# Kernel optimization log

Hardware: AMD Instinct MI355X
Metric: run time of the kernel (lower is better)

The kernel has to match this reference:

```python
import jax, jax.numpy as jnp
import numpy as np

N, E = 50000, 400000
HID, HT = 128, 128
HEADS, C = 4, 128  # TransformerConv heads=4, out_channels=hidden_X


def setup_inputs() -> dict:
    key = jax.random.key(0)
    ks = jax.random.split(key, 16)
    s = lambda k, shape, fan: jax.random.normal(k, shape, jnp.float32) / np.sqrt(fan)
    return {
        "edge_index": jax.random.randint(ks[0], (2, E), 0, N, dtype=jnp.int32),
        "h_X": jax.random.normal(ks[1], (N, HID), jnp.float32),
        "h_t": jax.random.normal(ks[2], (1, HT), jnp.float32),
        # TransformerConv params: lin_query/key/value: (HID -> HEADS*C), lin_skip: (HID -> C)
        "Wq": s(ks[3], (HID, HEADS * C), HID), "bq": jnp.zeros((HEADS * C,), jnp.float32),
        "Wk": s(ks[4], (HID, HEADS * C), HID), "bk": jnp.zeros((HEADS * C,), jnp.float32),
        "Wv": s(ks[5], (HID, HEADS * C), HID), "bv": jnp.zeros((HEADS * C,), jnp.float32),
        "Wskip": s(ks[6], (HID, C), HID), "bskip": jnp.zeros((C,), jnp.float32),
        # update_X: Linear(HID+HT -> HID), LayerNorm(HID)
        "Wup": s(ks[7], (HID + HT, HID), HID + HT), "bup": jnp.zeros((HID,), jnp.float32),
        "gamma": jnp.ones((HID,), jnp.float32), "beta": jnp.zeros((HID,), jnp.float32),
    }


def transformer_conv(h_X, edge_index, Wq, bq, Wk, bk, Wv, bv, Wskip, bskip):
    n = h_X.shape[0]
    src, dst = edge_index[0], edge_index[1]  # messages flow src -> dst
    q = (h_X @ Wq + bq).reshape(n, HEADS, C)
    k = (h_X @ Wk + bk).reshape(n, HEADS, C)
    v = (h_X @ Wv + bv).reshape(n, HEADS, C)
    # per-edge attention scores [E, H]
    score = jnp.einsum('ehc,ehc->eh', q[dst], k[src]) / np.sqrt(C)
    # segment softmax over incoming edges of each destination node
    m = jax.ops.segment_max(score, dst, num_segments=n)          # [N, H]
    ex = jnp.exp(score - m[dst])                                 # [E, H]
    denom = jax.ops.segment_sum(ex, dst, num_segments=n)        # [N, H]
    alpha = ex / denom[dst]                                      # [E, H]
    agg = jax.ops.segment_sum(alpha[..., None] * v[src], dst, num_segments=n)  # [N, H, C]
    out = agg.mean(axis=1)                                       # concat=False -> mean over heads
    return out + h_X @ Wskip + bskip                             # root_weight=True


def reference(edge_index, h_X, h_t, Wq, bq, Wk, bk, Wv, bv, Wskip, bskip,
              Wup, bup, gamma, beta):
    n = h_X.shape[0]
    h_att = transformer_conv(h_X, edge_index, Wq, bq, Wk, bk, Wv, bv, Wskip, bskip)
    h_t_exp = jnp.broadcast_to(h_t, (n, h_t.shape[1]))
    h = jnp.concatenate([h_att, h_t_exp], axis=1)
    h = jax.nn.relu(h @ Wup + bup)
    # LayerNorm (eps=1e-5); Dropout is identity in eval
    mu = h.mean(axis=-1, keepdims=True)
    var = ((h - mu) ** 2).mean(axis=-1, keepdims=True)
    return (h - mu) / jnp.sqrt(var + 1e-5) * gamma + beta
```

## Files before the change

### kernel.cpp

```cpp
#include <hip/hip_runtime.h>

typedef unsigned short u16;
typedef unsigned int   u32;

#define HID   128
#define HEADS 4
#define CH    128
#define HC    512
#define UT    32

typedef __bf16 bf16x8v __attribute__((ext_vector_type(8)));
typedef float  f32x4v  __attribute__((ext_vector_type(4)));
union FragU { uint4 u; bf16x8v b; };

static __device__ __forceinline__ float bf2f(u16 u) {
  union { u32 u; float f; } x;
  x.u = ((u32)u) << 16;
  return x.f;
}
static __device__ __forceinline__ u16 f2bf(float f) {
  union { float f; u32 u; } x;
  x.f = f;
  u32 r = x.u + 0x7fffu + ((x.u >> 16) & 1u);
  return (u16)(r >> 16);
}

__global__ void zero_kernel(int* p, int n) {
  int i = blockIdx.x * 256 + threadIdx.x;
  if (i < n) p[i] = 0;
}

__global__ void hist_kernel(const int* dst_idx, int* deg, int E) {
  int e = blockIdx.x * 256 + threadIdx.x;
  if (e < E) atomicAdd(&deg[dst_idx[e]], 1);
}

__global__ void blocksum_kernel(const int* deg, int* bsums, int n) {
  __shared__ int buf[256];
  int i = blockIdx.x * 256 + threadIdx.x;
  int v = 0;
  if (i < n) v = deg[i];
  buf[threadIdx.x] = v;
  __syncthreads();
  for (int off = 128; off > 0; off >>= 1) {
    if (threadIdx.x < off) buf[threadIdx.x] += buf[threadIdx.x + off];
    __syncthreads();
  }
  if (threadIdx.x == 0) bsums[blockIdx.x] = buf[0];
}

__global__ void scanb_kernel(const int* bsums, int* boffs, int nb) {
  __shared__ int buf[256];
  __shared__ int carry_s;
  int tid = threadIdx.x;
  if (tid == 0) carry_s = 0;
  __syncthreads();
  for (int base = 0; base < nb; base += 256) {
    int i = base + tid;
    int v = 0;
    if (i < nb) v = bsums[i];
    buf[tid] = v;
    __syncthreads();
    for (int off = 1; off < 256; off <<= 1) {
      int t = 0;
      if (tid >= off) t = buf[tid - off];
      __syncthreads();
      buf[tid] += t;
      __syncthreads();
    }
    int incl = buf[tid] + carry_s;
    if (i < nb) boffs[i] = incl - v;
    __syncthreads();
    if (tid == 255) carry_s = incl;
    __syncthreads();
  }
}

__global__ void scanfinal_kernel(const int* deg, const int* boffs,
                                 int* row_ptr, int* cursor, int n) {
  __shared__ int buf[256];
  int tid = threadIdx.x;
  int i = blockIdx.x * 256 + tid;
  int v = 0;
  if (i < n) v = deg[i];
  buf[tid] = v;
  __syncthreads();
  for (int off = 1; off < 256; off <<= 1) {
    int t = 0;
    if (tid >= off) t = buf[tid - off];
    __syncthreads();
    buf[tid] += t;
    __syncthreads();
  }
  int incl = buf[tid] + boffs[blockIdx.x];
  if (i < n) {
    row_ptr[i + 1] = incl;
    cursor[i] = incl - v;
  }
  if (i == 0) row_ptr[0] = 0;
}

__global__ void scatter_kernel(const int* src_idx, const int* dst_idx,
                               int* cursor, int* col, int E) {
  int e = blockIdx.x * 256 + threadIdx.x;
  if (e < E) {
    int pos = atomicAdd(&cursor[dst_idx[e]], 1);
    col[pos] = src_idx[e];
  }
}

__global__ void packH_kernel(const float* __restrict__ hX,
                             u16* __restrict__ hpack, int N, int total) {
  int i = blockIdx.x * 256 + threadIdx.x;
  if (i >= total) return;
  int j = i & 7;
  int lane = (i >> 3) & 63;
  int kc = (i >> 9) & 3;
  int ntile = i >> 11;
  int node = ntile * 16 + (lane & 15);
  int k = kc * 32 + (lane >> 4) * 8 + j;
  float v = (node < N) ? hX[(size_t)node * HID + k] : 0.f;
  hpack[i] = f2bf(v);
}

__global__ void packW_kernel(const float* __restrict__ WA,
                             const float* __restrict__ WB, int colsA, int ldA,
                             int ldB, u16* __restrict__ Wp, int total) {
  int i = blockIdx.x * 256 + threadIdx.x;
  if (i >= total) return;
  int j = i & 7;
  int lane = (i >> 3) & 63;
  int kc = (i >> 9) & 3;
  int ct = i >> 11;
  int n = ct * 16 + (lane & 15);
  int k = kc * 32 + (lane >> 4) * 8 + j;
  float w = (n < colsA) ? WA[(size_t)k * ldA + n]
                        : WB[(size_t)k * ldB + (n - colsA)];
  Wp[i] = f2bf(w);
}

__global__ __launch_bounds__(256) void mfma_proj_kernel(
    const u16* __restrict__ hpack, const u16* __restrict__ Wp,
    const float* __restrict__ biasLo, const float* __restrict__ biasHi,
    u16* __restrict__ outLo, u16* __restrict__ outHiB,
    float* __restrict__ outHiF, int hiIsF32, int N) {
  int t = threadIdx.x;
  int wv = t >> 6;
  int L = t & 63;
  int ct = blockIdx.y * 4 + wv;
  int nt0 = blockIdx.x * 4;

  f32x4v acc[4];
  for (int mt = 0; mt < 4; ++mt) acc[mt] = (f32x4v){0.f, 0.f, 0.f, 0.f};

  const u16* wb = Wp + (size_t)ct * 2048;
  const u16* hb = hpack + (size_t)nt0 * 2048;

  for (int kc = 0; kc < 4; ++kc) {
    FragU bf;
    bf.u = *(const uint4*)(wb + kc * 512 + L * 8);
    for (int mt = 0; mt < 4; ++mt) {
      FragU af;
      af.u = *(const uint4*)(hb + mt * 2048 + kc * 512 + L * 8);
      acc[mt] =
          __builtin_amdgcn_mfma_f32_16x16x32_bf16(af.b, bf.b, acc[mt], 0, 0, 0);
    }
  }

  int colq = L & 15;
  int quad = L >> 4;
  int n = ct * 16 + colq;
  float bias = (n < 512) ? biasLo[n] : biasHi[n - 512];
  for (int mt = 0; mt < 4; ++mt) {
    for (int rg = 0; rg < 4; ++rg) {
      int node = (nt0 + mt) * 16 + quad * 4 + rg;
      if (node < N) {
        float val = acc[mt][rg] + bias;
        if (n < 512) {
          outLo[(size_t)node * HC + n] = f2bf(val);
        } else if (hiIsF32) {
          outHiF[(size_t)node * HID + (n - 512)] = val;
        } else {
          outHiB[(size_t)node * HC + (n - 512)] = f2bf(val);
        }
      }
    }
  }
}

__global__ void score_kernel(const u16* qb, const u16* kb, const int* row_ptr,
                             const int* col_src, float* scores, int N) {
  int node = blockIdx.x * 4 + (threadIdx.x >> 6);
  if (node >= N) return;
  int lane = threadIdx.x & 63;
  int head = lane >> 4;
  int r = lane & 15;
  int foff = head * CH + r * 8;

  float qf[8];
  {
    uint4 raw = *(const uint4*)(qb + (size_t)node * HC + foff);
    qf[0] = bf2f((u16)(raw.x & 0xffffu));
    qf[1] = bf2f((u16)(raw.x >> 16));
    qf[2] = bf2f((u16)(raw.y & 0xffffu));
    qf[3] = bf2f((u16)(raw.y >> 16));
    qf[4] = bf2f((u16)(raw.z & 0xffffu));
    qf[5] = bf2f((u16)(raw.z >> 16));
    qf[6] = bf2f((u16)(raw.w & 0xffffu));
    qf[7] = bf2f((u16)(raw.w >> 16));
  }

  int e0 = row_ptr[node];
  int e1 = row_ptr[node + 1];
  for (int e = e0; e < e1; ++e) {
    int s = col_src[e];
    uint4 raw = *(const uint4*)(kb + (size_t)s * HC + foff);
    float p = 0.f;
    p = fmaf(bf2f((u16)(raw.x & 0xffffu)), qf[0], p);
    p = fmaf(bf2f((u16)(raw.x >> 16)),     qf[1], p);
    p = fmaf(bf2f((u16)(raw.y & 0xffffu)), qf[2], p);
    p = fmaf(bf2f((u16)(raw.y >> 16)),     qf[3], p);
    p = fmaf(bf2f((u16)(raw.z & 0xffffu)), qf[4], p);
    p = fmaf(bf2f((u16)(raw.z >> 16)),     qf[5], p);
    p = fmaf(bf2f((u16)(raw.w & 0xffffu)), qf[6], p);
    p = fmaf(bf2f((u16)(raw.w >> 16)),     qf[7], p);
    p += __shfl_xor(p, 1);
    p += __shfl_xor(p, 2);
    p += __shfl_xor(p, 4);
    p += __shfl_xor(p, 8);
    if (r == 0) scores[(size_t)e * HEADS + head] = p * 0.08838834764831845f;
  }
}

__global__ void attn_kernel(const float* scores, const u16* vb,
                            const int* row_ptr, const int* col_src,
                            float* out, int N) {
  int node = blockIdx.x * 4 + (threadIdx.x >> 6);
  if (node >= N) return;
  int lane = threadIdx.x & 63;
  int head = lane >> 4;
  int r = lane & 15;
  int foff = head * CH + r * 8;

  float m = -3.402823466e38f;
  float l = 0.f;
  float acc[8];
  for (int j = 0; j < 8; ++j) acc[j] = 0.f;

  int e0 = row_ptr[node];
  int e1 = row_ptr[node + 1];
  for (int e = e0; e < e1; ++e) {
    float sc = scores[(size_t)e * HEADS + head];
    int s = col_src[e];
    uint4 raw = *(const uint4*)(vb + (size_t)s * HC + foff);
    float vf[8];
    vf[0] = bf2f((u16)(raw.x & 0xffffu));
    vf[1] = bf2f((u16)(raw.x >> 16));
    vf[2] = bf2f((u16)(raw.y & 0xffffu));
    vf[3] = bf2f((u16)(raw.y >> 16));
    vf[4] = bf2f((u16)(raw.z & 0xffffu));
    vf[5] = bf2f((u16)(raw.z >> 16));
    vf[6] = bf2f((u16)(raw.w & 0xffffu));
    vf[7] = bf2f((u16)(raw.w >> 16));
    float mnew = fmaxf(m, sc);
    float scale = expf(m - mnew);
    float pe = expf(sc - mnew);
    l = l * scale + pe;
    for (int j = 0; j < 8; ++j) acc[j] = fmaf(acc[j], scale, pe * vf[j]);
    m = mnew;
  }

  float inv = 0.f;
  if (l > 0.f) inv = 1.0f / l;
  float val[8];
  for (int j = 0; j < 8; ++j) {
    float x = acc[j] * inv;
    x += __shfl_xor(x, 16);
    x += __shfl_xor(x, 32);
    val[j] = x * 0.25f;
  }

  if (head == 0) {
    float* p = out + (size_t)node * HID + r * 8;
    float4 a = *(const float4*)(p);
    float4 b = *(const float4*)(p + 4);
    a.x += val[0]; a.y += val[1]; a.z += val[2]; a.w += val[3];
    b.x += val[4]; b.y += val[5]; b.z += val[6]; b.w += val[7];
    *(float4*)(p) = a;
    *(float4*)(p + 4) = b;
  }
}

__global__ void cvec_kernel(const float* h_t, const float* Wup,
                            const float* bup, float* cvec) {
  int c = threadIdx.x;
  float acc = bup[c];
  for (int k = 0; k < 128; ++k)
    acc = fmaf(h_t[k], Wup[(size_t)(128 + k) * 128 + c], acc);
  cvec[c] = acc;
}

__global__ __launch_bounds__(256) void ATTLayer_19396072308956_kernel(
    float* out, const float* __restrict__ Wup, const float* __restrict__ cvec,
    const float* __restrict__ gamma, const float* __restrict__ beta, int N) {
  __shared__ float Wl[64 * 128];
  __shared__ float Hl[UT * 128];
  int t = threadIdx.x;
  int n0 = blockIdx.x * UT;

  for (int i = t * 4; i < UT * 128; i += 1024) {
    int node = n0 + (i >> 7);
    float4 v;
    if (node < N) {
      v = *(const float4*)(out + (size_t)node * HID + (i & 127));
    } else {
      v.x = 0.f; v.y = 0.f; v.z = 0.f; v.w = 0.f;
    }
    *(float4*)(Hl + i) = v;
  }

  int wv = t >> 6;
  int r = t & 63;
  int c0 = 2 * r;
  float2 cv = *(const float2*)(cvec + c0);
  float a0[8];
  float a1[8];
  for (int j = 0; j < 8; ++j) {
    a0[j] = cv.x;
    a1[j] = cv.y;
  }

  for (int ph = 0; ph < 2; ++ph) {
    __syncthreads();
    for (int i = t * 4; i < 64 * 128; i += 1024) {
      *(float4*)(Wl + i) = *(const float4*)(Wup + (size_t)ph * 64 * 128 + i);
    }
    __syncthreads();
    const float* hbase = Hl + (wv * 8) * 128 + ph * 64;
#pragma unroll 8
    for (int k = 0; k < 64; ++k) {
      float2 w2 = *(const float2*)(Wl + k * 128 + c0);
      for (int j = 0; j < 8; ++j) {
        float h = hbase[j * 128 + k];
        a0[j] = fmaf(h, w2.x, a0[j]);
        a1[j] = fmaf(h, w2.y, a1[j]);
      }
    }
  }

  float2 g = *(const float2*)(gamma + c0);
  float2 b = *(const float2*)(beta + c0);
  for (int j = 0; j < 8; ++j) {
    int node = n0 + wv * 8 + j;
    float r0 = fmaxf(a0[j], 0.f);
    float r1 = fmaxf(a1[j], 0.f);
    float s = r0 + r1;
    for (int msk = 1; msk < 64; msk <<= 1) s += __shfl_xor(s, msk);
    float mean = s * (1.0f / 128.0f);
    float d0 = r0 - mean;
    float d1 = r1 - mean;
    float sq = d0 * d0 + d1 * d1;
    for (int msk = 1; msk < 64; msk <<= 1) sq += __shfl_xor(sq, msk);
    float rstd = rsqrtf(sq * (1.0f / 128.0f) + 1e-5f);
    if (node < N) {
      float2 o;
      o.x = d0 * rstd * g.x + b.x;
      o.y = d1 * rstd * g.y + b.y;
      *(float2*)(out + (size_t)node * HID + c0) = o;
    }
  }
}

extern "C" void kernel_launch(void* const* d_in, const int* in_sizes, int n_in,
                              void* d_out, int out_size, void* d_ws,
                              size_t ws_size, hipStream_t stream) {
  (void)n_in;
  (void)out_size;
  (void)ws_size;

  const int* edge_index = (const int*)d_in[0];
  const float* hX    = (const float*)d_in[1];
  const float* h_t   = (const float*)d_in[2];
  const float* Wq    = (const float*)d_in[3];
  const float* bq    = (const float*)d_in[4];
  const float* Wk    = (const float*)d_in[5];
  const float* bk    = (const float*)d_in[6];
  const float* Wv    = (const float*)d_in[7];
  const float* bv    = (const float*)d_in[8];
  const float* Wskip = (const float*)d_in[9];
  const float* bskip = (const float*)d_in[10];
  const float* Wup   = (const float*)d_in[11];
  const float* bup   = (const float*)d_in[12];
  const float* gamma = (const float*)d_in[13];
  const float* beta  = (const float*)d_in[14];

  const int E = in_sizes[0] / 2;
  const int N = in_sizes[1] / HID;
  const int* src_idx = edge_index;
  const int* dst_idx = edge_index + E;
  const int NB = (N + 255) / 256;
  const int NTILES = (N + 15) / 16;
  const int NTILES4 = ((NTILES + 3) / 4) * 4;

  char* w = (char*)d_ws;
  size_t off = 0;
  float* cvec = (float*)(w + off);
  off += 256 * 4;
  int* deg = (int*)(w + off);
  off += ((size_t)N * 4 + 255) / 256 * 256;
  int* row_ptr = (int*)(w + off);
  off += ((size_t)(N + 1) * 4 + 255) / 256 * 256;
  int* cursor = (int*)(w + off);
  off += ((size_t)N * 4 + 255) / 256 * 256;
  int* bsums = (int*)(w + off);
  off += ((size_t)NB * 4 + 255) / 256 * 256;
  int* boffs = (int*)(w + off);
  off += ((size_t)NB * 4 + 255) / 256 * 256;
  int* col = (int*)(w + off);
  off += ((size_t)E * 4 + 255) / 256 * 256;
  float* scores = (float*)(w + off);
  off += ((size_t)E * HEADS * 4 + 255) / 256 * 256;
  u16* hpack = (u16*)(w + off);
  off += ((size_t)NTILES4 * 2048 * 2 + 255) / 256 * 256;
  u16* Wp1 = (u16*)(w + off);
  off += ((size_t)128 * 1024 * 2 + 255) / 256 * 256;
  u16* Wp2 = (u16*)(w + off);
  off += ((size_t)128 * 640 * 2 + 255) / 256 * 256;
  u16* bigA = (u16*)(w + off);
  off += ((size_t)N * HC * 2 + 255) / 256 * 256;
  u16* bigB = (u16*)(w + off);
  off += ((size_t)N * HC * 2 + 255) / 256 * 256;

  float* out = (float*)d_out;

  zero_kernel<<<NB, 256, 0, stream>>>(deg, N);
  hist_kernel<<<(E + 255) / 256, 256, 0, stream>>>(dst_idx, deg, E);
  blocksum_kernel<<<NB, 256, 0, stream>>>(deg, bsums, N);
  scanb_kernel<<<1, 256, 0, stream>>>(bsums, boffs, NB);
  scanfinal_kernel<<<NB, 256, 0, stream>>>(deg, boffs, row_ptr, cursor, N);
  scatter_kernel<<<(E + 255) / 256, 256, 0, stream>>>(src_idx, dst_idx, cursor,
                                                      col, E);

  int totH = NTILES4 * 2048;
  packH_kernel<<<(totH + 255) / 256, 256, 0, stream>>>(hX, hpack, N, totH);
  packW_kernel<<<(128 * 1024 + 255) / 256, 256, 0, stream>>>(
      Wq, Wk, 512, HC, HC, Wp1, 128 * 1024);
  packW_kernel<<<(128 * 640 + 255) / 256, 256, 0, stream>>>(
      Wv, Wskip, 512, HC, HID, Wp2, 128 * 640);

  cvec_kernel<<<1, 128, 0, stream>>>(h_t, Wup, bup, cvec);

  mfma_proj_kernel<<<dim3(NTILES4 / 4, 16), 256, 0, stream>>>(
      hpack, Wp1, bq, bk, bigA, bigB, (float*)nullptr, 0, N);

  score_kernel<<<(N + 3) / 4, 256, 0, stream>>>(bigA, bigB, row_ptr, col,
                                                scores, N);

  mfma_proj_kernel<<<dim3(NTILES4 / 4, 10), 256, 0, stream>>>(
      hpack, Wp2, bv, bskip, bigA, (u16*)nullptr, out, 1, N);

  attn_kernel<<<(N + 3) / 4, 256, 0, stream>>>(scores, bigA, row_ptr, col, out,
                                               N);

  ATTLayer_19396072308956_kernel<<<(N + UT - 1) / UT, 256, 0, stream>>>(
      out, Wup, cvec, gamma, beta, N);
}
```

Measured before the change: 461.9 us.

## Fuse score and softmax-aggregation into one edge pass with separate V buffer

Adds a fused attention kernel that computes q·k scores and the online-softmax aggregation of v in a single pass over each node's incoming edges, processing two edges per iteration. V is written to a new workspace buffer so Q/K stay live. This drops the per-edge score array write/read and the second walk over the CSR structure. The fused path is used only if the workspace is large enough, and exp is switched to the fast __expf in both paths.

```diff
diff --git a/kernel.cpp b/kernel.cpp
--- a/kernel.cpp
+++ b/kernel.cpp
@@ -23,6 +23,17 @@
   x.f = f;
   u32 r = x.u + 0x7fffu + ((x.u >> 16) & 1u);
   return (u16)(r >> 16);
+}
+
+static __device__ __forceinline__ void unpack8(uint4 raw, float* dst) {
+  dst[0] = bf2f((u16)(raw.x & 0xffffu));
+  dst[1] = bf2f((u16)(raw.x >> 16));
+  dst[2] = bf2f((u16)(raw.y & 0xffffu));
+  dst[3] = bf2f((u16)(raw.y >> 16));
+  dst[4] = bf2f((u16)(raw.z & 0xffffu));
+  dst[5] = bf2f((u16)(raw.z >> 16));
+  dst[6] = bf2f((u16)(raw.w & 0xffffu));
+  dst[7] = bf2f((u16)(raw.w >> 16));
 }
 
 __global__ void zero_kernel(int* p, int n) {
@@ -188,6 +199,112 @@
   }
 }
 
+__global__ void fused_attn_kernel(const u16* __restrict__ qb,
+                                  const u16* __restrict__ kb,
+                                  const u16* __restrict__ vb,
+                                  const int* __restrict__ row_ptr,
+                                  const int* __restrict__ col_src,
+                                  float* out, int N) {
+  int node = blockIdx.x * 4 + (threadIdx.x >> 6);
+  if (node >= N) return;
+  int lane = threadIdx.x & 63;
+  int head = lane >> 4;
+  int r = lane & 15;
+  int foff = head * CH + r * 8;
+  const float sscale = 0.08838834764831845f;
+
+  float qf[8];
+  unpack8(*(const uint4*)(qb + (size_t)node * HC + foff), qf);
+
+  float m = -3.402823466e38f;
+  float l = 0.f;
+  float acc[8];
+  for (int j = 0; j < 8; ++j) acc[j] = 0.f;
+
+  int e0 = row_ptr[node];
+  int e1 = row_ptr[node + 1];
+  int e = e0;
+  for (; e + 2 <= e1; e += 2) {
+    int s0 = col_src[e];
+    int s1 = col_src[e + 1];
+    uint4 k0 = *(const uint4*)(kb + (size_t)s0 * HC + foff);
+    uint4 k1 = *(const uint4*)(kb + (size_t)s1 * HC + foff);
+    uint4 v0 = *(const uint4*)(vb + (size_t)s0 * HC + foff);
+    uint4 v1 = *(const uint4*)(vb + (size_t)s1 * HC + foff);
+    float k0f[8], k1f[8];
+    unpack8(k0, k0f);
+    unpack8(k1, k1f);
+    float p0 = 0.f, p1 = 0.f;
+    for (int j = 0; j < 8; ++j) {
+      p0 = fmaf(k0f[j], qf[j], p0);
+      p1 = fmaf(k1f[j], qf[j], p1);
+    }
+    p0 += __shfl_xor(p0, 1);
+    p1 += __shfl_xor(p1, 1);
+    p0 += __shfl_xor(p0, 2);
+    p1 += __shfl_xor(p1, 2);
+    p0 += __shfl_xor(p0, 4);
+    p1 += __shfl_xor(p1, 4);
+    p0 += __shfl_xor(p0, 8);
+    p1 += __shfl_xor(p1, 8);
+    float sc0 = p0 * sscale;
+    float sc1 = p1 * sscale;
+    float mnew = fmaxf(m, fmaxf(sc0, sc1));
+    float so = __expf(m - mnew);
+    float pe0 = __expf(sc0 - mnew);
+    float pe1 = __expf(sc1 - mnew);
+    l = l * so + pe0 + pe1;
+    float v0f[8], v1f[8];
+    unpack8(v0, v0f);
+    unpack8(v1, v1f);
+    for (int j = 0; j < 8; ++j)
+      acc[j] = fmaf(acc[j], so, fmaf(pe0, v0f[j], pe1 * v1f[j]));
+    m = mnew;
+  }
+  if (e < e1) {
+    int s0 = col_src[e];
+    uint4 k0 = *(const uint4*)(kb + (size_t)s0 * HC + foff);
+    uint4 v0 = *(const uint4*)(vb + (size_t)s0 * HC + foff);
+    float k0f[8];
+    unpack8(k0, k0f);
+    float p0 = 0.f;
+    for (int j = 0; j < 8; ++j) p0 = fmaf(k0f[j], qf[j], p0);
+    p0 += __shfl_xor(p0, 1);
+    p0 += __shfl_xor(p0, 2);
+    p0 += __shfl_xor(p0, 4);
+    p0 += __shfl_xor(p0, 8);
+    float sc0 = p0 * sscale;
+    float mnew = fmaxf(m, sc0);
+    float so = __expf(m - mnew);
+    float pe0 = __expf(sc0 - mnew);
+    l = l * so + pe0;
+    float v0f[8];
+    unpack8(v0, v0f);
+    for (int j = 0; j < 8; ++j) acc[j] = fmaf(acc[j], so, pe0 * v0f[j]);
+    m = mnew;
+  }
+
+  float inv = 0.f;
+  if (l > 0.f) inv = 1.0f / l;
+  float val[8];
+  for (int j = 0; j < 8; ++j) {
+    float x = acc[j] * inv;
+    x += __shfl_xor(x, 16);
+    x += __shfl_xor(x, 32);
+    val[j] = x * 0.25f;
+  }
+
+  if (head == 0) {
+    float* p = out + (size_t)node * HID + r * 8;
+    float4 a = *(const float4*)(p);
+    float4 b = *(const float4*)(p + 4);
+    a.x += val[0]; a.y += val[1]; a.z += val[2]; a.w += val[3];
+    b.x += val[4]; b.y += val[5]; b.z += val[6]; b.w += val[7];
+    *(float4*)(p) = a;
+    *(float4*)(p + 4) = b;
+  }
+}
+
 __global__ void score_kernel(const u16* qb, const u16* kb, const int* row_ptr,
                              const int* col_src, float* scores, int N) {
   int node = blockIdx.x * 4 + (threadIdx.x >> 6);
@@ -198,32 +315,17 @@
   int foff = head * CH + r * 8;
 
   float qf[8];
-  {
-    uint4 raw = *(const uint4*)(qb + (size_t)node * HC + foff);
-    qf[0] = bf2f((u16)(raw.x & 0xffffu));
-    qf[1] = bf2f((u16)(raw.x >> 16));
-    qf[2] = bf2f((u16)(raw.y & 0xffffu));
-    qf[3] = bf2f((u16)(raw.y >> 16));
-    qf[4] = bf2f((u16)(raw.z & 0xffffu));
-    qf[5] = bf2f((u16)(raw.z >> 16));
-    qf[6] = bf2f((u16)(raw.w & 0xffffu));
-    qf[7] = bf2f((u16)(raw.w >> 16));
-  }
+  unpack8(*(const uint4*)(qb + (size_t)node * HC + foff), qf);
 
   int e0 = row_ptr[node];
   int e1 = row_ptr[node + 1];
   for (int e = e0; e < e1; ++e) {
     int s = col_src[e];
     uint4 raw = *(const uint4*)(kb + (size_t)s * HC + foff);
+    float kf[8];
+    unpack8(raw, kf);
     float p = 0.f;
-    p = fmaf(bf2f((u16)(raw.x & 0xffffu)), qf[0], p);
-    p = fmaf(bf2f((u16)(raw.x >> 16)),     qf[1], p);
-    p = fmaf(bf2f((u16)(raw.y & 0xffffu)), qf[2], p);
-    p = fmaf(bf2f((u16)(raw.y >> 16)),     qf[3], p);
-    p = fmaf(bf2f((u16)(raw.z & 0xffffu)), qf[4], p);
-    p = fmaf(bf2f((u16)(raw.z >> 16)),     qf[5], p);
-    p = fmaf(bf2f((u16)(raw.w & 0xffffu)), qf[6], p);
-    p = fmaf(bf2f((u16)(raw.w >> 16)),     qf[7], p);
+    for (int j = 0; j < 8; ++j) p = fmaf(kf[j], qf[j], p);
     p += __shfl_xor(p, 1);
     p += __shfl_xor(p, 2);
     p += __shfl_xor(p, 4);
@@ -254,17 +356,10 @@
     int s = col_src[e];
     uint4 raw = *(const uint4*)(vb + (size_t)s * HC + foff);
     float vf[8];
-    vf[0] = bf2f((u16)(raw.x & 0xffffu));
-    vf[1] = bf2f((u16)(raw.x >> 16));
-    vf[2] = bf2f((u16)(raw.y & 0xffffu));
-    vf[3] = bf2f((u16)(raw.y >> 16));
-    vf[4] = bf2f((u16)(raw.z & 0xffffu));
-    vf[5] = bf2f((u16)(raw.z >> 16));
-    vf[6] = bf2f((u16)(raw.w & 0xffffu));
-    vf[7] = bf2f((u16)(raw.w >> 16));
+    unpack8(raw, vf);
     float mnew = fmaxf(m, sc);
-    float scale = expf(m - mnew);
-    float pe = expf(sc - mnew);
+    float scale = __expf(m - mnew);
+    float pe = __expf(sc - mnew);
     l = l * scale + pe;
     for (int j = 0; j < 8; ++j) acc[j] = fmaf(acc[j], scale, pe * vf[j]);
     m = mnew;
@@ -376,7 +471,6 @@
                               size_t ws_size, hipStream_t stream) {
   (void)n_in;
   (void)out_size;
-  (void)ws_size;
 
   const int* edge_index = (const int*)d_in[0];
   const float* hX    = (const float*)d_in[1];
@@ -430,6 +524,9 @@
   off += ((size_t)N * HC * 2 + 255) / 256 * 256;
   u16* bigB = (u16*)(w + off);
   off += ((size_t)N * HC * 2 + 255) / 256 * 256;
+  u16* bigC = (u16*)(w + off);
+  size_t off_fused = off + ((size_t)N * HC * 2 + 255) / 256 * 256;
+  const int use_fused = (ws_size >= off_fused) ? 1 : 0;
 
   float* out = (float*)d_out;
 
@@ -453,14 +550,19 @@
   mfma_proj_kernel<<<dim3(NTILES4 / 4, 16), 256, 0, stream>>>(
       hpack, Wp1, bq, bk, bigA, bigB, (float*)nullptr, 0, N);
 
-  score_kernel<<<(N + 3) / 4, 256, 0, stream>>>(bigA, bigB, row_ptr, col,
-                                                scores, N);
-
-  mfma_proj_kernel<<<dim3(NTILES4 / 4, 10), 256, 0, stream>>>(
-      hpack, Wp2, bv, bskip, bigA, (u16*)nullptr, out, 1, N);
-
-  attn_kernel<<<(N + 3) / 4, 256, 0, stream>>>(scores, bigA, row_ptr, col, out,
-                                               N);
+  if (use_fused) {
+    mfma_proj_kernel<<<dim3(NTILES4 / 4, 10), 256, 0, stream>>>(
+        hpack, Wp2, bv, bskip, bigC, (u16*)nullptr, out, 1, N);
+    fused_attn_kernel<<<(N + 3) / 4, 256, 0, stream>>>(bigA, bigB, bigC,
+                                                       row_ptr, col, out, N);
+  } else {
+    score_kernel<<<(N + 3) / 4, 256, 0, stream>>>(bigA, bigB, row_ptr, col,
+                                                  scores, N);
+    mfma_proj_kernel<<<dim3(NTILES4 / 4, 10), 256, 0, stream>>>(
+        hpack, Wp2, bv, bskip, bigA, (u16*)nullptr, out, 1, N);
+    attn_kernel<<<(N + 3) / 4, 256, 0, stream>>>(scores, bigA, row_ptr, col,
+                                                 out, N);
+  }
 
   ATTLayer_19396072308956_kernel<<<(N + UT - 1) / UT, 256, 0, stream>>>(
       out, Wup, cvec, gamma, beta, N);
```

Result: faster. 447.9 us (-3.0%).
